# Kernel tuning notes

Hardware: AMD Instinct MI355X
Metric: run time of the kernel (lower is better)

## Reference

```python
import jax, jax.numpy as jnp
import numpy as np

KB, KI = 6, 0   # kernel quantizer: quantized_bits(6, 0, alpha=1)
BB, BI = 6, 0   # bias quantizer:   quantized_bits(6, 0, alpha=1)
AB, AI = 6, 0   # activation:       quantized_relu(6, 0)


def _round_ste(p):
    # straight-through round (QKeras _round_through); tf.round and jnp.round
    # both round half-to-even
    return p + jax.lax.stop_gradient(jnp.round(p) - p)


def quantized_bits(x, bits, integer):
    # QKeras quantized_bits with keep_negative=1, symmetric=0, alpha=1
    m = float(2 ** (bits - 1))      # non-sign levels
    m_i = float(2 ** integer)
    p = x * (m / m_i)
    return (m_i / m) * jnp.clip(_round_ste(p), -m, m - 1.0)


def quantized_relu(x, bits, integer):
    # QKeras quantized_relu with negative_slope=0, use_sigmoid=0
    m = float(2 ** bits)
    m_i = float(2 ** integer)
    p = x * (m / m_i)
    return (m_i / m) * jnp.clip(_round_ste(p), 0.0, m - 1.0)


def setup_inputs() -> dict:
    key = jax.random.key(0)
    ks = jax.random.split(key, 9)
    dims = [128, 1024, 2048, 4096, 4096]
    inp = {"x": jax.random.normal(ks[0], (8192, dims[0]), dtype=jnp.float32)}
    for i in range(4):
        fan_in, fan_out = dims[i], dims[i + 1]
        scale = np.sqrt(2.0 / (fan_in + fan_out))  # glorot-ish scale
        inp[f"W{i}"] = jax.random.normal(ks[1 + 2 * i], (fan_in, fan_out), dtype=jnp.float32) * scale
        inp[f"b{i}"] = jax.random.normal(ks[2 + 2 * i], (fan_out,), dtype=jnp.float32) * 0.01
    return inp


def reference(x, W0, b0, W1, b1, W2, b2, W3, b3):
    Ws = [W0, W1, W2, W3]
    bs = [b0, b1, b2, b3]
    h = x
    for i in range(4):
        wq = quantized_bits(Ws[i], KB, KI)
        bq = quantized_bits(bs[i], BB, BI)
        h = jnp.dot(h, wq) + bq
        if i != 3:  # last layer has activation=None
            h = quantized_relu(h, AB, AI)
    return h
```

## Files before the change

### kernel.cpp

```cpp
#include <hip/hip_runtime.h>
#include <stdint.h>

typedef int v4i __attribute__((ext_vector_type(4)));

__device__ __forceinline__ float qlevel(float x) {
  float p = rintf(x * 32.0f);
  return fminf(fmaxf(p, -32.0f), 31.0f);
}

__device__ __forceinline__ int8_t qrelu_level(float p) {
  int q = (int)rintf(p);
  q = q < 0 ? 0 : (q > 63 ? 63 : q);
  return (int8_t)q;
}

__device__ __forceinline__ void async16(const void* g, void* l) {
  __builtin_amdgcn_global_load_lds(
      (const __attribute__((address_space(1))) void*)g,
      (__attribute__((address_space(3))) void*)l, 16, 0, 0);
}

__global__ __launch_bounds__(256) void quant_w0_k(const float* __restrict__ W,
                                                  int8_t* __restrict__ wq) {
  int i = blockIdx.x * 256 + threadIdx.x;
  float4 v = ((const float4*)W)[i];
  char4 c;
  c.x = (int8_t)(int)qlevel(v.x);
  c.y = (int8_t)(int)qlevel(v.y);
  c.z = (int8_t)(int)qlevel(v.z);
  c.w = (int8_t)(int)qlevel(v.w);
  ((char4*)wq)[i] = c;
}

__global__ __launch_bounds__(256) void quantT_k(const float* __restrict__ W,
                                                int8_t* __restrict__ wt,
                                                int K, int N) {
  const int t = threadIdx.x;
  const int l = t & 63;
  const int kc = t >> 6;
  const int k0 = blockIdx.y * 64 + kc * 16;
  const int n = blockIdx.x * 64 + l;
  union { int8_t b[16]; int4 v; } u;
#pragma unroll
  for (int j = 0; j < 16; ++j)
    u.b[j] = (int8_t)(int)qlevel(W[(size_t)(k0 + j) * N + n]);
  *(int4*)&wt[(size_t)n * K + k0] = u.v;
}

__global__ __launch_bounds__(256) void quant_bias_k(
    const float* __restrict__ b0, const float* __restrict__ b1,
    const float* __restrict__ b2, const float* __restrict__ b3,
    float* __restrict__ o0, float* __restrict__ o1,
    float* __restrict__ o2, float* __restrict__ o3) {
  int i = blockIdx.x * 256 + threadIdx.x;
  if (i < 1024) o0[i] = qlevel(b0[i]);
  if (i < 2048) o1[i] = qlevel(b1[i]);
  o2[i] = qlevel(b2[i]);
  o3[i] = qlevel(b3[i]);
}

__global__ __launch_bounds__(256) void layer0_k(const float* __restrict__ x,
                                                const int8_t* __restrict__ w0q,
                                                const float* __restrict__ bint,
                                                int8_t* __restrict__ a1) {
  const int K = 128, N = 1024;
  __shared__ float xs[64][132];
  __shared__ int8_t wsm[128][64];
  const int tid = threadIdx.x;
  const int m0 = blockIdx.y * 64;
  const int n0 = blockIdx.x * 64;
#pragma unroll
  for (int i = 0; i < 8; ++i) {
    int idx = tid + 256 * i;
    int row = idx >> 5, c4 = idx & 31;
    float4 v = *(const float4*)(x + (size_t)(m0 + row) * K + c4 * 4);
    *(float4*)&xs[row][c4 * 4] = v;
  }
#pragma unroll
  for (int i = 0; i < 8; ++i) {
    int idx = tid + 256 * i;
    int k = idx >> 4, c4 = idx & 15;
    *(int*)&wsm[k][c4 * 4] = *(const int*)(w0q + (size_t)k * N + n0 + c4 * 4);
  }
  __syncthreads();
  const int ty = tid >> 4, tx = tid & 15;
  float acc[4][4] = {};
  for (int k4 = 0; k4 < K; k4 += 4) {
    float xr[4][4];
#pragma unroll
    for (int i = 0; i < 4; ++i) {
      float4 v = *(const float4*)&xs[ty * 4 + i][k4];
      xr[i][0] = v.x; xr[i][1] = v.y; xr[i][2] = v.z; xr[i][3] = v.w;
    }
#pragma unroll
    for (int kk = 0; kk < 4; ++kk) {
      char4 cv = *(const char4*)&wsm[k4 + kk][tx * 4];
      float w0 = (float)cv.x, w1 = (float)cv.y, w2 = (float)cv.z, w3 = (float)cv.w;
#pragma unroll
      for (int i = 0; i < 4; ++i) {
        acc[i][0] = fmaf(xr[i][kk], w0, acc[i][0]);
        acc[i][1] = fmaf(xr[i][kk], w1, acc[i][1]);
        acc[i][2] = fmaf(xr[i][kk], w2, acc[i][2]);
        acc[i][3] = fmaf(xr[i][kk], w3, acc[i][3]);
      }
    }
  }
  const int n = n0 + tx * 4;
  float b0v = 2.0f * bint[n + 0], b1v = 2.0f * bint[n + 1];
  float b2v = 2.0f * bint[n + 2], b3v = 2.0f * bint[n + 3];
#pragma unroll
  for (int i = 0; i < 4; ++i) {
    int m = m0 + ty * 4 + i;
    char4 o;
    o.x = qrelu_level(2.0f * acc[i][0] + b0v);
    o.y = qrelu_level(2.0f * acc[i][1] + b1v);
    o.z = qrelu_level(2.0f * acc[i][2] + b2v);
    o.w = qrelu_level(2.0f * acc[i][3] + b3v);
    *(char4*)&a1[(size_t)m * 1024 + n] = o;
  }
}

template <bool FINAL>
__global__ __launch_bounds__(256) void gemm_i8(const int8_t* __restrict__ A,
                                               const int8_t* __restrict__ BT,
                                               const float* __restrict__ bint,
                                               void* __restrict__ outp,
                                               int M, int N, int K) {
  __shared__ __align__(16) int8_t ldsA[2][64 * 128];
  __shared__ __align__(16) int8_t ldsB[2][64 * 128];
  const int tid = threadIdx.x;
  const int wid = tid >> 6;
  const int lane = tid & 63;
  const int wm = wid >> 1, wn = wid & 1;
  const int quad = lane >> 4, r = lane & 15;
  const int m0 = blockIdx.y * 128, n0 = blockIdx.x * 128;

  const int8_t* Ab = A + (size_t)m0 * K;
  const int8_t* Bb = BT + (size_t)n0 * K;

  const int srow = tid >> 2;
  const int sp = tid & 3;
  const int skc = (sp - (srow >> 1)) & 3;
  const int8_t* gA0 = Ab + (size_t)srow * K + skc * 16;
  const int8_t* gA1 = Ab + (size_t)(srow + 64) * K + skc * 16;
  const int8_t* gB0 = Bb + (size_t)srow * K + skc * 16;
  const int8_t* gB1 = Bb + (size_t)(srow + 64) * K + skc * 16;
  const int ldsOff0 = (wid * 64) * 16;
  const int ldsOff1 = (wid * 64 + 256) * 16;

  const int pfrag = (quad + (r >> 1)) & 3;

  v4i acc[4][4] = {};

  async16(gA0, &ldsA[0][ldsOff0]);
  async16(gA1, &ldsA[0][ldsOff1]);
  async16(gB0, &ldsB[0][ldsOff0]);
  async16(gB1, &ldsB[0][ldsOff1]);
  __syncthreads();

  for (int k0 = 0; k0 < K; k0 += 64) {
    const int p = (k0 >> 6) & 1;
    if (k0 + 64 < K) {
      async16(gA0 + k0 + 64, &ldsA[1 - p][ldsOff0]);
      async16(gA1 + k0 + 64, &ldsA[1 - p][ldsOff1]);
      async16(gB0 + k0 + 64, &ldsB[1 - p][ldsOff0]);
      async16(gB1 + k0 + 64, &ldsB[1 - p][ldsOff1]);
    }
    v4i af[4], bf[4];
#pragma unroll
    for (int mt = 0; mt < 4; ++mt)
      af[mt] = *(const v4i*)&ldsA[p][(wm * 64 + mt * 16 + r) * 64 + pfrag * 16];
#pragma unroll
    for (int nt = 0; nt < 4; ++nt)
      bf[nt] = *(const v4i*)&ldsB[p][(wn * 64 + nt * 16 + r) * 64 + pfrag * 16];
#pragma unroll
    for (int mt = 0; mt < 4; ++mt)
#pragma unroll
      for (int nt = 0; nt < 4; ++nt)
        acc[mt][nt] = __builtin_amdgcn_mfma_i32_16x16x64_i8(af[mt], bf[nt],
                                                            acc[mt][nt], 0, 0, 0);
    __syncthreads();
  }

  const int mbase = m0 + wm * 64;
  const int nbase = n0 + wn * 64;
  if (FINAL) {
    float* out = (float*)outp;
#pragma unroll
    for (int nt = 0; nt < 4; ++nt) {
      int n = nbase + nt * 16 + r;
      float bq = bint[n] * 0.03125f;
#pragma unroll
      for (int mt = 0; mt < 4; ++mt)
#pragma unroll
        for (int g = 0; g < 4; ++g) {
          int m = mbase + mt * 16 + quad * 4 + g;
          out[(size_t)m * N + n] = (float)acc[mt][nt][g] * (1.0f / 2048.0f) + bq;
        }
    }
  } else {
    int8_t* out = (int8_t*)outp;
#pragma unroll
    for (int nt = 0; nt < 4; ++nt) {
      int n = nbase + nt * 16 + r;
      float b2 = 2.0f * bint[n];
#pragma unroll
      for (int mt = 0; mt < 4; ++mt)
#pragma unroll
        for (int g = 0; g < 4; ++g) {
          int m = mbase + mt * 16 + quad * 4 + g;
          out[(size_t)m * N + n] =
              qrelu_level((float)acc[mt][nt][g] * 0.03125f + b2);
        }
    }
  }
}

extern "C" void kernel_launch(void* const* d_in, const int* in_sizes, int n_in,
                              void* d_out, int out_size, void* d_ws, size_t ws_size,
                              hipStream_t stream) {
  const float* x  = (const float*)d_in[0];
  const float* W0 = (const float*)d_in[1];
  const float* b0 = (const float*)d_in[2];
  const float* W1 = (const float*)d_in[3];
  const float* b1 = (const float*)d_in[4];
  const float* W2 = (const float*)d_in[5];
  const float* b2 = (const float*)d_in[6];
  const float* W3 = (const float*)d_in[7];
  const float* b3 = (const float*)d_in[8];

  uint8_t* ws = (uint8_t*)d_ws;
  int8_t* wq0 = (int8_t*)(ws + 0);
  int8_t* wt1 = (int8_t*)(ws + 131072);
  int8_t* wt2 = (int8_t*)(ws + 2228224);
  int8_t* wt3 = (int8_t*)(ws + 10616832);
  float*  bq0 = (float*)(ws + 27394048);
  float*  bq1 = (float*)(ws + 27398144);
  float*  bq2 = (float*)(ws + 27406336);
  float*  bq3 = (float*)(ws + 27422720);
  int8_t* a1  = (int8_t*)(ws + 27439104);
  int8_t* a2  = (int8_t*)(ws + 35827712);
  int8_t* a3  = (int8_t*)(ws + 52604928);

  quant_w0_k<<<128, 256, 0, stream>>>(W0, wq0);
  quantT_k<<<dim3(2048 / 64, 1024 / 64), 256, 0, stream>>>(W1, wt1, 1024, 2048);
  quantT_k<<<dim3(4096 / 64, 2048 / 64), 256, 0, stream>>>(W2, wt2, 2048, 4096);
  quantT_k<<<dim3(4096 / 64, 4096 / 64), 256, 0, stream>>>(W3, wt3, 4096, 4096);
  quant_bias_k<<<16, 256, 0, stream>>>(b0, b1, b2, b3, bq0, bq1, bq2, bq3);
  layer0_k<<<dim3(16, 128), 256, 0, stream>>>(x, wq0, bq0, a1);
  gemm_i8<false><<<dim3(16, 64), 256, 0, stream>>>(a1, wt1, bq1, a2, 8192, 2048, 1024);
  gemm_i8<false><<<dim3(32, 64), 256, 0, stream>>>(a2, wt2, bq2, a3, 8192, 4096, 2048);
  gemm_i8<true><<<dim3(32, 64), 256, 0, stream>>>(a3, wt3, bq3, d_out, 8192, 4096, 4096);
}
```

Baseline: 523.9 us.

## Enlarge int8 GEMM tile to 256x256 with 4-stage async LDS pipeline

Result: slower. 539.2 us (+2.9%).

```diff
diff --git a/kernel.cpp b/kernel.cpp
--- a/kernel.cpp
+++ b/kernel.cpp
@@ -121,19 +121,19 @@
 }
 
 template <bool FINAL>
-__global__ __launch_bounds__(256) void gemm_i8(const int8_t* __restrict__ A,
+__global__ __launch_bounds__(512) void gemm_i8(const int8_t* __restrict__ A,
                                                const int8_t* __restrict__ BT,
                                                const float* __restrict__ bint,
                                                void* __restrict__ outp,
                                                int M, int N, int K) {
-  __shared__ __align__(16) int8_t ldsA[2][64 * 128];
-  __shared__ __align__(16) int8_t ldsB[2][64 * 128];
+  __shared__ __align__(16) int8_t ldsA[4][256 * 64];
+  __shared__ __align__(16) int8_t ldsB[4][256 * 64];
   const int tid = threadIdx.x;
   const int wid = tid >> 6;
   const int lane = tid & 63;
-  const int wm = wid >> 1, wn = wid & 1;
+  const int wm = wid >> 2, wn = wid & 3;
   const int quad = lane >> 4, r = lane & 15;
-  const int m0 = blockIdx.y * 128, n0 = blockIdx.x * 128;
+  const int m0 = blockIdx.y * 256, n0 = blockIdx.x * 256;
 
   const int8_t* Ab = A + (size_t)m0 * K;
   const int8_t* Bb = BT + (size_t)n0 * K;
@@ -142,47 +142,90 @@
   const int sp = tid & 3;
   const int skc = (sp - (srow >> 1)) & 3;
   const int8_t* gA0 = Ab + (size_t)srow * K + skc * 16;
-  const int8_t* gA1 = Ab + (size_t)(srow + 64) * K + skc * 16;
+  const int8_t* gA1 = Ab + (size_t)(srow + 128) * K + skc * 16;
   const int8_t* gB0 = Bb + (size_t)srow * K + skc * 16;
-  const int8_t* gB1 = Bb + (size_t)(srow + 64) * K + skc * 16;
+  const int8_t* gB1 = Bb + (size_t)(srow + 128) * K + skc * 16;
   const int ldsOff0 = (wid * 64) * 16;
-  const int ldsOff1 = (wid * 64 + 256) * 16;
+  const int ldsOff1 = (512 + wid * 64) * 16;
 
   const int pfrag = (quad + (r >> 1)) & 3;
 
-  v4i acc[4][4] = {};
-
-  async16(gA0, &ldsA[0][ldsOff0]);
-  async16(gA1, &ldsA[0][ldsOff1]);
-  async16(gB0, &ldsB[0][ldsOff0]);
-  async16(gB1, &ldsB[0][ldsOff1]);
-  __syncthreads();
-
-  for (int k0 = 0; k0 < K; k0 += 64) {
-    const int p = (k0 >> 6) & 1;
-    if (k0 + 64 < K) {
-      async16(gA0 + k0 + 64, &ldsA[1 - p][ldsOff0]);
-      async16(gA1 + k0 + 64, &ldsA[1 - p][ldsOff1]);
-      async16(gB0 + k0 + 64, &ldsB[1 - p][ldsOff0]);
-      async16(gB1 + k0 + 64, &ldsB[1 - p][ldsOff1]);
-    }
-    v4i af[4], bf[4];
-#pragma unroll
-    for (int mt = 0; mt < 4; ++mt)
-      af[mt] = *(const v4i*)&ldsA[p][(wm * 64 + mt * 16 + r) * 64 + pfrag * 16];
-#pragma unroll
-    for (int nt = 0; nt < 4; ++nt)
-      bf[nt] = *(const v4i*)&ldsB[p][(wn * 64 + nt * 16 + r) * 64 + pfrag * 16];
-#pragma unroll
-    for (int mt = 0; mt < 4; ++mt)
-#pragma unroll
-      for (int nt = 0; nt < 4; ++nt)
-        acc[mt][nt] = __builtin_amdgcn_mfma_i32_16x16x64_i8(af[mt], bf[nt],
-                                                            acc[mt][nt], 0, 0, 0);
-    __syncthreads();
-  }
-
-  const int mbase = m0 + wm * 64;
+  v4i acc[8][4] = {};
+
+#define STAGE(buf, kt)                                   \
+  do {                                                   \
+    const int koff_ = (kt) * 64;                         \
+    async16(gA0 + koff_, &ldsA[buf][ldsOff0]);           \
+    async16(gA1 + koff_, &ldsA[buf][ldsOff1]);           \
+    async16(gB0 + koff_, &ldsB[buf][ldsOff0]);           \
+    async16(gB1 + koff_, &ldsB[buf][ldsOff1]);           \
+  } while (0)
+
+#define COMPUTE(pbuf)                                                         \
+  do {                                                                        \
+    const int8_t* La_ = &ldsA[pbuf][0];                                       \
+    const int8_t* Lb_ = &ldsB[pbuf][0];                                       \
+    v4i bf[4], af[4];                                                         \
+    _Pragma("unroll")                                                         \
+    for (int nt = 0; nt < 4; ++nt)                                            \
+      bf[nt] = *(const v4i*)&Lb_[(wn * 64 + nt * 16 + r) * 64 + pfrag * 16];  \
+    _Pragma("unroll")                                                         \
+    for (int mt = 0; mt < 4; ++mt)                                            \
+      af[mt] = *(const v4i*)&La_[(wm * 128 + mt * 16 + r) * 64 + pfrag * 16]; \
+    __builtin_amdgcn_s_setprio(1);                                            \
+    _Pragma("unroll")                                                         \
+    for (int mt = 0; mt < 4; ++mt)                                            \
+      _Pragma("unroll")                                                       \
+      for (int nt = 0; nt < 4; ++nt)                                          \
+        acc[mt][nt] = __builtin_amdgcn_mfma_i32_16x16x64_i8(                  \
+            af[mt], bf[nt], acc[mt][nt], 0, 0, 0);                            \
+    __builtin_amdgcn_s_setprio(0);                                            \
+    _Pragma("unroll")                                                         \
+    for (int mt = 0; mt < 4; ++mt)                                            \
+      af[mt] = *(const v4i*)&La_[(wm * 128 + 64 + mt * 16 + r) * 64 +         \
+                                 pfrag * 16];                                 \
+    __builtin_amdgcn_s_setprio(1);                                            \
+    _Pragma("unroll")                                                         \
+    for (int mt = 0; mt < 4; ++mt)                                            \
+      _Pragma("unroll")                                                       \
+      for (int nt = 0; nt < 4; ++nt)                                          \
+        acc[4 + mt][nt] = __builtin_amdgcn_mfma_i32_16x16x64_i8(              \
+            af[mt], bf[nt], acc[4 + mt][nt], 0, 0, 0);                        \
+    __builtin_amdgcn_s_setprio(0);                                            \
+  } while (0)
+
+  const int NT = K >> 6;
+
+  STAGE(0, 0);
+  STAGE(1, 1);
+  STAGE(2, 2);
+  STAGE(3, 3);
+  asm volatile("s_waitcnt vmcnt(12)" ::: "memory");
+  __builtin_amdgcn_s_barrier();
+
+  for (int t = 0; t < NT - 4; ++t) {
+    const int p = t & 3;
+    COMPUTE(p);
+    __builtin_amdgcn_s_barrier();
+    STAGE(p, t + 4);
+    asm volatile("s_waitcnt vmcnt(12)" ::: "memory");
+    __builtin_amdgcn_s_barrier();
+  }
+  COMPUTE((NT - 4) & 3);
+  asm volatile("s_waitcnt vmcnt(8)" ::: "memory");
+  __builtin_amdgcn_s_barrier();
+  COMPUTE((NT - 3) & 3);
+  asm volatile("s_waitcnt vmcnt(4)" ::: "memory");
+  __builtin_amdgcn_s_barrier();
+  COMPUTE((NT - 2) & 3);
+  asm volatile("s_waitcnt vmcnt(0)" ::: "memory");
+  __builtin_amdgcn_s_barrier();
+  COMPUTE((NT - 1) & 3);
+
+#undef STAGE
+#undef COMPUTE
+
+  const int mbase = m0 + wm * 128;
   const int nbase = n0 + wn * 64;
   if (FINAL) {
     float* out = (float*)outp;
@@ -191,7 +234,7 @@
       int n = nbase + nt * 16 + r;
       float bq = bint[n] * 0.03125f;
 #pragma unroll
-      for (int mt = 0; mt < 4; ++mt)
+      for (int mt = 0; mt < 8; ++mt)
 #pragma unroll
         for (int g = 0; g < 4; ++g) {
           int m = mbase + mt * 16 + quad * 4 + g;
@@ -205,7 +248,7 @@
       int n = nbase + nt * 16 + r;
       float b2 = 2.0f * bint[n];
 #pragma unroll
-      for (int mt = 0; mt < 4; ++mt)
+      for (int mt = 0; mt < 8; ++mt)
 #pragma unroll
         for (int g = 0; g < 4; ++g) {
           int m = mbase + mt * 16 + quad * 4 + g;
@@ -248,7 +291,10 @@
   quantT_k<<<dim3(4096 / 64, 4096 / 64), 256, 0, stream>>>(W3, wt3, 4096, 4096);
   quant_bias_k<<<16, 256, 0, stream>>>(b0, b1, b2, b3, bq0, bq1, bq2, bq3);
   layer0_k<<<dim3(16, 128), 256, 0, stream>>>(x, wq0, bq0, a1);
-  gemm_i8<false><<<dim3(16, 64), 256, 0, stream>>>(a1, wt1, bq1, a2, 8192, 2048, 1024);
-  gemm_i8<false><<<dim3(32, 64), 256, 0, stream>>>(a2, wt2, bq2, a3, 8192, 4096, 2048);
-  gemm_i8<true><<<dim3(32, 64), 256, 0, stream>>>(a3, wt3, bq3, d_out, 8192, 4096, 4096);
-}
+  gemm_i8<false><<<dim3(2048 / 256, 8192 / 256), 512, 0, stream>>>(
+      a1, wt1, bq1, a2, 8192, 2048, 1024);
+  gemm_i8<false><<<dim3(4096 / 256, 8192 / 256), 512, 0, stream>>>(
+      a2, wt2, bq2, a3, 8192, 4096, 2048);
+  gemm_i8<true><<<dim3(4096 / 256, 8192 / 256), 512, 0, stream>>>(
+      a3, wt3, bq3, d_out, 8192, 4096, 4096);
+}
```
